# Kernel tuning notes

Hardware: AMD Instinct MI355X
Metric: run time of the kernel (lower is better)

Reference implementation:

```python
import jax, jax.numpy as jnp
import numpy as np

B, N, F = 4, 256, 128
H = 256  # hidden width of readout MLP
OUT = 1


def setup_inputs() -> dict:
    key = jax.random.key(0)
    k_x, k_wp, k_w1, k_b1, k_w2, k_b2 = jax.random.split(key, 6)
    node_embeddings = jax.random.normal(k_x, (B, N, F), dtype=jnp.float32)
    # layer_pooled: Linear(F, F, bias=False); stored as [in, out]
    W_pool = jax.random.normal(k_wp, (F, F), dtype=jnp.float32) / np.sqrt(F)
    # readout layer 1: Linear(3F, H, bias=True)
    W1 = jax.random.normal(k_w1, (3 * F, H), dtype=jnp.float32) / np.sqrt(3 * F)
    b1 = jax.random.normal(k_b1, (H,), dtype=jnp.float32) * 0.01
    # readout layer 2: Linear(H, OUT, bias=True)
    W2 = jax.random.normal(k_w2, (H, OUT), dtype=jnp.float32) / np.sqrt(H)
    b2 = jax.random.normal(k_b2, (OUT,), dtype=jnp.float32) * 0.01
    return {"node_embeddings": node_embeddings, "W_pool": W_pool,
            "W1": W1, "b1": b1, "W2": W2, "b2": b2}


def reference(node_embeddings, W_pool, W1, b1, W2, b2):
    b, n, f = node_embeddings.shape
    # pooled context: mean over nodes, then Linear(F,F) (no bias)
    h_pooled = jnp.einsum('bf,fh->bh', node_embeddings.mean(axis=1), W_pool)  # [B,F]
    # pairwise grid: features[b,i,j] = relu(concat(h_pooled[b], x[b,i], x[b,j]))
    f_pooled = jnp.broadcast_to(h_pooled[:, None, None, :], (b, n, n, f))
    f_i = jnp.broadcast_to(node_embeddings[:, :, None, :], (b, n, n, f))  # f_expanded
    f_j = jnp.broadcast_to(node_embeddings[:, None, :, :], (b, n, n, f))  # f_expanded_diff
    features = jax.nn.relu(jnp.concatenate([f_pooled, f_i, f_j], axis=-1))  # [B,N,N,3F]
    h = jax.nn.relu(jnp.einsum('bijk,kh->bijh', features, W1) + b1)  # [B,N,N,H]
    out = jnp.einsum('bijh,ho->bijo', h, W2) + b2  # [B,N,N,OUT]
    return out
```

## Files before the change

kernel.cpp:

```cpp
#include <hip/hip_runtime.h>
#include <hip/hip_bf16.h>

#define B 4
#define N 256
#define F 128
#define H 256

__global__ __launch_bounds__(256) void kAW(
    const float* __restrict__ x, const float* __restrict__ Wp,
    const float* __restrict__ W1, const float* __restrict__ b1,
    float* __restrict__ ub, float* __restrict__ A, float* __restrict__ W) {
  __shared__ float xr[2][F];
  const int blk = blockIdx.x;
  const int b = blk >> 7;
  const int i0 = (blk & 127) * 2;
  const int t = threadIdx.x;

  {
    const int r = t >> 7, f = t & 127;
    xr[r][f] = fmaxf(x[(b * N + i0 + r) * F + f], 0.f);
  }
  __syncthreads();

  float a0 = 0.f, a1 = 0.f, w0 = 0.f, w1 = 0.f;
  const float* W1i = W1 + F * H;
  const float* W1j = W1 + 2 * F * H;
#pragma unroll 8
  for (int f = 0; f < F; ++f) {
    const float wi = W1i[f * H + t];
    const float wj = W1j[f * H + t];
    const float x0 = xr[0][f];
    const float x1 = xr[1][f];
    a0 = fmaf(x0, wi, a0);
    a1 = fmaf(x1, wi, a1);
    w0 = fmaf(x0, wj, w0);
    w1 = fmaf(x1, wj, w1);
  }
  A[(b * N + i0) * H + t] = a0;
  A[(b * N + i0 + 1) * H + t] = a1;
  W[(b * N + i0) * H + t] = w0;
  W[(b * N + i0 + 1) * H + t] = w1;

  if (blk < B) {
    __shared__ float4 red4[256];
    __shared__ float xm_s[F];
    __shared__ float rp_s[F];
    __shared__ float part[256];
    const int pb = blk;
    const float4* xb4 = (const float4*)(x + pb * N * F);
    float4 acc = make_float4(0.f, 0.f, 0.f, 0.f);
#pragma unroll 8
    for (int k = 0; k < 32; ++k) {
      const float4 v = xb4[t + 256 * k];
      acc.x += v.x; acc.y += v.y; acc.z += v.z; acc.w += v.w;
    }
    red4[t] = acc;
    __syncthreads();
    if (t < 32) {
      float4 s = red4[t];
#pragma unroll
      for (int m = 1; m < 8; ++m) {
        const float4 v = red4[t + 32 * m];
        s.x += v.x; s.y += v.y; s.z += v.z; s.w += v.w;
      }
      const float inv = 1.f / (float)N;
      xm_s[4 * t + 0] = s.x * inv;
      xm_s[4 * t + 1] = s.y * inv;
      xm_s[4 * t + 2] = s.z * inv;
      xm_s[4 * t + 3] = s.w * inv;
    }
    __syncthreads();
    {
      const int lo = t & 127, kh = t >> 7;
      float p = 0.f;
      const int k0 = kh * 64;
#pragma unroll 8
      for (int kk = 0; kk < 64; ++kk) {
        const int k = k0 + kk;
        p = fmaf(xm_s[k], Wp[k * F + lo], p);
      }
      part[t] = p;
    }
    __syncthreads();
    if (t < 128) rp_s[t] = fmaxf(part[t] + part[t + 128], 0.f);
    __syncthreads();
    {
      float u = b1[t];
#pragma unroll 8
      for (int k = 0; k < F; ++k) u = fmaf(rp_s[k], W1[k * H + t], u);
      ub[pb * H + t] = u;
    }
  }
}

#define SA 34
#define SW 17
__global__ __launch_bounds__(256) void kPair(
    const float* __restrict__ A, const float* __restrict__ W,
    const float* __restrict__ ub, const float* __restrict__ W2,
    const float* __restrict__ b2, float* __restrict__ out) {
  __shared__ float aT[256 * SA];
  __shared__ float wT[256 * SW];
  __shared__ float w2s[256];

  const int b = blockIdx.z;
  const int i0 = blockIdx.y * 32;
  const int j0 = blockIdx.x * 16;
  const int t = threadIdx.x;

  w2s[t] = W2[t];
  const float ubv = ub[b * H + t];

  const float* Ab = A + (b * N + i0) * H;
#pragma unroll 8
  for (int r = 0; r < 32; ++r)
    aT[t * SA + r] = Ab[r * H + t] + ubv;

  const float* Wb = W + (b * N + j0) * H;
#pragma unroll 8
  for (int r = 0; r < 16; ++r)
    wT[t * SW + r] = Wb[r * H + t];
  __syncthreads();

  const int ti = t >> 3;
  const int tj = t & 7;
  float acc0 = 0.f, acc1 = 0.f;
#pragma unroll 8
  for (int h = 0; h < 256; ++h) {
    const float a  = aT[h * SA + ti];
    const float v0 = wT[h * SW + 2 * tj];
    const float v1 = wT[h * SW + 2 * tj + 1];
    const float w2 = w2s[h];
    acc0 = fmaf(fmaxf(a + v0, 0.f), w2, acc0);
    acc1 = fmaf(fmaxf(a + v1, 0.f), w2, acc1);
  }

  const float bb = b2[0];
  float* o = out + (b * N + i0 + ti) * N + j0 + 2 * tj;
  o[0] = acc0 + bb;
  o[1] = acc1 + bb;
}

extern "C" void kernel_launch(void* const* d_in, const int* in_sizes, int n_in,
                              void* d_out, int out_size, void* d_ws, size_t ws_size,
                              hipStream_t stream) {
  const float* x  = (const float*)d_in[0];
  const float* Wp = (const float*)d_in[1];
  const float* W1 = (const float*)d_in[2];
  const float* b1 = (const float*)d_in[3];
  const float* W2 = (const float*)d_in[4];
  const float* b2 = (const float*)d_in[5];
  float* out = (float*)d_out;

  float* ws = (float*)d_ws;
  float* ub = ws;
  float* A  = ub + B * H;
  float* W  = A + B * N * H;

  kAW<<<dim3(B * N / 2), dim3(256), 0, stream>>>(x, Wp, W1, b1, ub, A, W);
  kPair<<<dim3(N / 16, N / 32, B), dim3(256), 0, stream>>>(A, W, ub, W2, b2, out);
}
```

Measured before the change: 89.61 us.

## Store pair-kernel shared tiles row-major as float4 for vectorized LDS reads

The pair kernel now keeps A and W tiles in shared memory in row-major float4 layout with padded rows, replacing the transposed scalar layout. Global loads become float4 and coalesced, and the inner loop reads float4 from LDS, handling four hidden units per step. Threads now take j columns tj and tj+8 instead of two adjacent columns. The aim is fewer LDS instructions and cheaper tile loads; bank conflicts from the float4 row stride and higher register use are possible costs.

Result: no change. 88.96 us (-0.7%).

```diff
diff --git a/kernel.cpp b/kernel.cpp
--- a/kernel.cpp
+++ b/kernel.cpp
@@ -93,52 +93,70 @@
   }
 }
 
-#define SA 34
-#define SW 17
+#define SROW 65
 __global__ __launch_bounds__(256) void kPair(
     const float* __restrict__ A, const float* __restrict__ W,
     const float* __restrict__ ub, const float* __restrict__ W2,
     const float* __restrict__ b2, float* __restrict__ out) {
-  __shared__ float aT[256 * SA];
-  __shared__ float wT[256 * SW];
-  __shared__ float w2s[256];
+  __shared__ float4 aS[32 * SROW];
+  __shared__ float4 wS[16 * SROW];
+  __shared__ float4 w2s[64];
 
   const int b = blockIdx.z;
   const int i0 = blockIdx.y * 32;
   const int j0 = blockIdx.x * 16;
   const int t = threadIdx.x;
 
-  w2s[t] = W2[t];
-  const float ubv = ub[b * H + t];
+  const int c = t & 63;
+  const int rp = t >> 6;
 
-  const float* Ab = A + (b * N + i0) * H;
-#pragma unroll 8
-  for (int r = 0; r < 32; ++r)
-    aT[t * SA + r] = Ab[r * H + t] + ubv;
+  if (t < 64) w2s[t] = ((const float4*)W2)[t];
 
-  const float* Wb = W + (b * N + j0) * H;
-#pragma unroll 8
-  for (int r = 0; r < 16; ++r)
-    wT[t * SW + r] = Wb[r * H + t];
+  const float4 ubv = ((const float4*)(ub + b * H))[c];
+
+  const float4* A4 = (const float4*)(A + (size_t)(b * N + i0) * H);
+#pragma unroll
+  for (int p = 0; p < 8; ++p) {
+    const int r = rp + 4 * p;
+    float4 v = A4[r * 64 + c];
+    v.x += ubv.x; v.y += ubv.y; v.z += ubv.z; v.w += ubv.w;
+    aS[r * SROW + c] = v;
+  }
+  const float4* W4 = (const float4*)(W + (size_t)(b * N + j0) * H);
+#pragma unroll
+  for (int p = 0; p < 4; ++p) {
+    const int r = rp + 4 * p;
+    wS[r * SROW + c] = W4[r * 64 + c];
+  }
   __syncthreads();
 
   const int ti = t >> 3;
   const int tj = t & 7;
+  const float4* ap  = aS + ti * SROW;
+  const float4* wp0 = wS + tj * SROW;
+  const float4* wp1 = wS + (tj + 8) * SROW;
+
   float acc0 = 0.f, acc1 = 0.f;
-#pragma unroll 8
-  for (int h = 0; h < 256; ++h) {
-    const float a  = aT[h * SA + ti];
-    const float v0 = wT[h * SW + 2 * tj];
-    const float v1 = wT[h * SW + 2 * tj + 1];
-    const float w2 = w2s[h];
-    acc0 = fmaf(fmaxf(a + v0, 0.f), w2, acc0);
-    acc1 = fmaf(fmaxf(a + v1, 0.f), w2, acc1);
+#pragma unroll 4
+  for (int hq = 0; hq < 64; ++hq) {
+    const float4 av = ap[hq];
+    const float4 w0 = wp0[hq];
+    const float4 w1 = wp1[hq];
+    const float4 w2 = w2s[hq];
+    acc0 = fmaf(fmaxf(av.x + w0.x, 0.f), w2.x, acc0);
+    acc0 = fmaf(fmaxf(av.y + w0.y, 0.f), w2.y, acc0);
+    acc0 = fmaf(fmaxf(av.z + w0.z, 0.f), w2.z, acc0);
+    acc0 = fmaf(fmaxf(av.w + w0.w, 0.f), w2.w, acc0);
+    acc1 = fmaf(fmaxf(av.x + w1.x, 0.f), w2.x, acc1);
+    acc1 = fmaf(fmaxf(av.y + w1.y, 0.f), w2.y, acc1);
+    acc1 = fmaf(fmaxf(av.z + w1.z, 0.f), w2.z, acc1);
+    acc1 = fmaf(fmaxf(av.w + w1.w, 0.f), w2.w, acc1);
   }
 
   const float bb = b2[0];
-  float* o = out + (b * N + i0 + ti) * N + j0 + 2 * tj;
-  o[0] = acc0 + bb;
-  o[1] = acc1 + bb;
+  float* o = out + (size_t)(b * N + i0 + ti) * N + j0;
+  o[tj] = acc0 + bb;
+  o[tj + 8] = acc1 + bb;
 }
 
 extern "C" void kernel_launch(void* const* d_in, const int* in_sizes, int n_in,
```
